# Performance work log

Measured on AMD Instinct MI355X. Metric: run time of the kernel, lower is better.

Reference implementation:

```python
import jax, jax.numpy as jnp
import numpy as np

SCALE_BASE = 512.0
GAMMA = 0.96875

def xpos(x, downscale=False):
    # x: (B, L, d). XPOS = rotary embedding with exponential position-dependent scale.
    B, L, d = x.shape
    half = d // 2
    scale_vec = (jnp.arange(0, d, 2, dtype=jnp.float32) + 0.4 * d) / (1.4 * d)  # (half,)
    pos = jnp.arange(L, dtype=jnp.float32)
    scale = scale_vec[None, :] ** (pos[:, None] / SCALE_BASE)  # (L, half)
    if downscale:
        scale = 1.0 / scale
    inv_freq = 1.0 / (10000.0 ** (jnp.arange(half, dtype=jnp.float32) / half))
    sinusoid = pos[:, None] * inv_freq[None, :]  # (L, half)
    sin_s = jnp.repeat(jnp.sin(sinusoid) * scale, 2, axis=-1)  # duplicate_interleave -> (L, d)
    cos_s = jnp.repeat(jnp.cos(sinusoid) * scale, 2, axis=-1)
    x1, x2 = x[..., ::2], x[..., 1::2]
    rot = jnp.stack((-x2, x1), axis=-1).reshape(x.shape)  # rotate_every_two
    return x * cos_s + rot * sin_s

def decay_mask(L, gamma):
    n = jnp.arange(L)[:, None]
    m = jnp.arange(L)[None, :]
    diff = n - m
    expo = jnp.where(diff >= 0, diff, 0).astype(jnp.float32)
    return jnp.where(diff >= 0, gamma ** expo, 0.0)  # (L, L) causal decay

def setup_inputs() -> dict:
    key = jax.random.key(0)
    kx, kq, kk, kv = jax.random.split(key, 4)
    B, L, H = 4, 2048, 1024
    hs = 1024  # head_size == v_dim
    X = jax.random.normal(kx, (B, L, H), dtype=jnp.float32)
    W_Q = jax.random.normal(kq, (H, hs), dtype=jnp.float32) / H
    W_K = jax.random.normal(kk, (H, hs), dtype=jnp.float32) / H
    W_V = jax.random.normal(kv, (H, hs), dtype=jnp.float32) / H
    return {"X": X, "W_Q": W_Q, "W_K": W_K, "W_V": W_V}

def reference(X, W_Q, W_K, W_V):
    L = X.shape[1]
    Q = xpos(X @ W_Q)
    K = xpos(X @ W_K, downscale=True)
    V = X @ W_V
    D = decay_mask(L, GAMMA)
    ret = jnp.einsum('bnd,bmd->bnm', Q, K) * D[None]  # (B, L, L)
    return ret @ V
```

## Files before the change

### kernel.cpp

```cpp
#include <hip/hip_runtime.h>
#include <cmath>

typedef __attribute__((ext_vector_type(8))) short short8;
typedef __attribute__((ext_vector_type(4))) short short4v;
typedef __attribute__((ext_vector_type(16))) float floatx16;
typedef __attribute__((ext_vector_type(4))) int int4v;
typedef unsigned short ushort_t;

#define LSEQ   2048
#define DMODEL 1024
#define BM 128
#define BN 128
#define BK 64
#define TPAD 136

#define L2GAMMA (-0.045803595f)
#define L2E4_512 (0.0259525632f)

__device__ __forceinline__ ushort_t f2b(float x) {
    union { float f; unsigned u; } v; v.f = x;
    unsigned r = v.u + 0x7fffu + ((v.u >> 16) & 1u);
    return (ushort_t)(r >> 16);
}

#define GLOAD_LDS16(gptr, lptr)                                                     \
    __builtin_amdgcn_global_load_lds(                                               \
        (const __attribute__((address_space(1))) unsigned int*)(gptr),              \
        (__attribute__((address_space(3))) unsigned int*)(lptr), 16, 0, 0)

#define DSR(d, a, o) \
    asm volatile("ds_read_b128 %0, %1 offset:" o : "=v"(d) : "v"(a))

__device__ __forceinline__ short8 as_s8(int4v v) {
    return __builtin_bit_cast(short8, v);
}
#define MFMA_B16 __builtin_amdgcn_mfma_f32_32x32x16_bf16

__device__ __forceinline__ void gemm_core(
    const ushort_t* __restrict__ Ag, int lda, int aRow0,
    const ushort_t* __restrict__ Bg, int ldb, int bRow0,
    int kDepth, ushort_t* As, ushort_t* Bs, floatx16 acc[2][2])
{
    const int tid  = threadIdx.x;
    const int wave = tid >> 6, lane = tid & 63;
    const int wm = wave >> 1, wn = wave & 1;
    const int l31 = lane & 31, half = lane >> 5;
    const int srow = lane >> 3;
    const int scol = ((lane & 7) ^ srow) * 8;

    const ushort_t* ap[4];
    const ushort_t* bp[4];
    #pragma unroll
    for (int L = 0; L < 4; ++L) {
        int r = (wave * 4 + L) * 8 + srow;
        ap[L] = Ag + (size_t)(aRow0 + r) * lda + scol;
        bp[L] = Bg + (size_t)(bRow0 + r) * ldb + scol;
    }
    const int ldst = (lane >> 3) * BK + (lane & 7) * 8;

    for (int k0 = 0; k0 < kDepth; k0 += BK) {
        __syncthreads();
        #pragma unroll
        for (int L = 0; L < 4; ++L) {
            GLOAD_LDS16(ap[L], As + (wave * 4 + L) * (8 * BK) + ldst);
            GLOAD_LDS16(bp[L], Bs + (wave * 4 + L) * (8 * BK) + ldst);
            ap[L] += BK; bp[L] += BK;
        }
        __syncthreads();

        #pragma unroll
        for (int ks = 0; ks < 4; ++ks) {
            const int ch = ((ks * 2 + half) ^ (l31 & 7)) * 8;
            short8 a0 = *(const short8*)(As + (wm * 64      + l31) * BK + ch);
            short8 a1 = *(const short8*)(As + (wm * 64 + 32 + l31) * BK + ch);
            short8 b0 = *(const short8*)(Bs + (wn * 64      + l31) * BK + ch);
            short8 b1 = *(const short8*)(Bs + (wn * 64 + 32 + l31) * BK + ch);
            acc[0][0] = MFMA_B16(a0, b0, acc[0][0], 0, 0, 0);
            acc[0][1] = MFMA_B16(a0, b1, acc[0][1], 0, 0, 0);
            acc[1][0] = MFMA_B16(a1, b0, acc[1][0], 0, 0, 0);
            acc[1][1] = MFMA_B16(a1, b1, acc[1][1], 0, 0, 0);
        }
    }
}

__global__ __launch_bounds__(256) void xpos_table_kernel(float2* __restrict__ T)
{
    int idx = blockIdx.x * 256 + threadIdx.x;
    int l = idx & 2047;
    int p = (idx >> 11) & 511;
    int mode = idx >> 20;
    float sv = (2.0f * (float)p + 409.6f) * (1.0f / 1433.6f);
    float coeff = log2f(sv) * (1.0f / 512.0f) + L2GAMMA;
    float invf = exp2f(-(float)p * L2E4_512);
    float lf = (float)l;
    float s, c;
    sincosf(lf * invf, &s, &c);
    float g = exp2f((mode == 0 ? lf : -lf) * coeff);
    T[idx] = make_float2(c * g, s * g);
}

__global__ __launch_bounds__(256) void cast_x_kernel(
    const float4* __restrict__ X, short4v* __restrict__ Xb, int n4)
{
    int i = blockIdx.x * 256 + threadIdx.x;
    if (i < n4) {
        float4 v = X[i];
        short4v o;
        o.x = (short)f2b(v.x); o.y = (short)f2b(v.y);
        o.z = (short)f2b(v.z); o.w = (short)f2b(v.w);
        Xb[i] = o;
    }
}

__global__ __launch_bounds__(256) void wtrans_kernel(
    const float* __restrict__ Wq, const float* __restrict__ Wk,
    const float* __restrict__ Wv, ushort_t* __restrict__ Wt)
{
    const float* W = blockIdx.z == 0 ? Wq : blockIdx.z == 1 ? Wk : Wv;
    ushort_t* O = Wt + (size_t)blockIdx.z * (DMODEL * DMODEL);
    __shared__ float t[32][33];
    const int x = threadIdx.x & 31, y = (threadIdx.x >> 5) * 4;
    const int k0 = blockIdx.y * 32, n0 = blockIdx.x * 32;
    #pragma unroll
    for (int j = 0; j < 4; ++j)
        t[y + j][x] = W[(size_t)(k0 + y + j) * DMODEL + n0 + x];
    __syncthreads();
    #pragma unroll
    for (int j = 0; j < 4; ++j)
        O[(size_t)(n0 + y + j) * DMODEL + k0 + x] = f2b(t[x][y + j]);
}

__global__ __launch_bounds__(256, 4) void qkv_kernel(
    const ushort_t* __restrict__ Xb, const ushort_t* __restrict__ Wt,
    const float2* __restrict__ Tab,
    ushort_t* __restrict__ Q, ushort_t* __restrict__ Ko, ushort_t* __restrict__ Vt)
{
    __shared__ ushort_t smem[128 * TPAD];
    ushort_t* As = smem;
    ushort_t* Bs = smem + BM * BK;

    const int lin = blockIdx.x;
    const int inner = lin & 63;
    const int sup = lin >> 6;
    const int c = (sup % 3) * 8 + (inner & 7);
    const int r = (sup / 3) * 8 + (inner >> 3);
    const int mode = c >> 3;
    const int c0 = (c & 7) * BN;
    const int row0 = r * BM;

    floatx16 acc[2][2] = {};
    gemm_core(Xb, DMODEL, row0,
              Wt + (size_t)mode * (DMODEL * DMODEL), DMODEL, c0,
              DMODEL, As, Bs, acc);

    const int wave = threadIdx.x >> 6, lane = threadIdx.x & 63;
    const int wm = wave >> 1, wn = wave & 1;
    const int l31 = lane & 31, half = lane >> 5;
    const int rBase = row0 + wm * 64 + 4 * half;
    const int cBase = c0 + wn * 64 + l31;

    if (mode == 2) {
        const int colL0 = wn * 64 + l31;
        const int rowL0 = wm * 64 + 4 * half;
        __syncthreads();
        #pragma unroll
        for (int mi = 0; mi < 2; ++mi)
            #pragma unroll
            for (int ni = 0; ni < 2; ++ni)
                #pragma unroll
                for (int rg = 0; rg < 4; ++rg) {
                    short4v pk;
                    pk.x = (short)f2b(acc[mi][ni][rg * 4 + 0]);
                    pk.y = (short)f2b(acc[mi][ni][rg * 4 + 1]);
                    pk.z = (short)f2b(acc[mi][ni][rg * 4 + 2]);
                    pk.w = (short)f2b(acc[mi][ni][rg * 4 + 3]);
                    *(short4v*)(smem + (colL0 + ni * 32) * TPAD
                                     + rowL0 + mi * 32 + 8 * rg) = pk;
                }
        __syncthreads();
        const int t = threadIdx.x;
        const int colV = c0 + (t >> 1);
        const int lhalf = (t & 1) * 64;
        const int b = row0 >> 11, lpos0 = (row0 & 2047) + lhalf;
        #pragma unroll
        for (int i = 0; i < 8; ++i) {
            short8 vv = *(const short8*)(smem + (t >> 1) * TPAD + lhalf + i * 8);
            *(short8*)(Vt + (size_t)b * (LSEQ * DMODEL)
                          + (size_t)colV * LSEQ + lpos0 + i * 8) = vv;
        }
    } else {
        ushort_t* O = (mode == 0) ? Q : Ko;
        const float2* Tm = Tab + (size_t)mode * (512 * 2048);
        #pragma unroll
        for (int ni = 0; ni < 2; ++ni) {
            int col = cBase + ni * 32;
            const float2* tp = Tm + ((size_t)(col >> 1) << 11);
            #pragma unroll
            for (int mi = 0; mi < 2; ++mi)
                #pragma unroll
                for (int rg = 0; rg < 4; ++rg) {
                    int l0 = (rBase + mi * 32 + 8 * rg) & 2047;
                    float4 t01 = *(const float4*)(tp + l0);
                    float4 t23 = *(const float4*)(tp + l0 + 2);
                    float cs[8] = {t01.x, t01.y, t01.z, t01.w,
                                   t23.x, t23.y, t23.z, t23.w};
                    #pragma unroll
                    for (int q = 0; q < 4; ++q) {
                        int row = rBase + mi * 32 + 8 * rg + q;
                        float cc = cs[2 * q], ss = cs[2 * q + 1];
                        float v  = acc[mi][ni][rg * 4 + q];
                        float pv = __shfl_xor(v, 1);
                        float res = (lane & 1) ? fmaf(v, cc, pv * ss)
                                               : fmaf(v, cc, -pv * ss);
                        O[(size_t)row * DMODEL + col] = f2b(res);
                    }
                }
        }
    }
}

__global__ __launch_bounds__(512, 2) void qkv256_kernel(
    const ushort_t* __restrict__ Xb, const ushort_t* __restrict__ Wt,
    const float2* __restrict__ Tab,
    ushort_t* __restrict__ Q, ushort_t* __restrict__ Ko, ushort_t* __restrict__ Vt)
{
    extern __shared__ ushort_t smem[];
    const int tid  = threadIdx.x;
    const int wave = tid >> 6, lane = tid & 63;
    const int wm = wave >> 2, wn = wave & 3;
    const int l31 = lane & 31, half = lane >> 5;
    const int xl  = l31 & 7;

    const int nwg = gridDim.x;
    const int cpx = nwg >> 3;
    const int orig = blockIdx.x;
    const int wg = (orig & 7) * cpx + (orig >> 3);
    const int sup = wg >> 4, inner = wg & 15;
    const int ct = (sup % 3) * 4 + (inner & 3);
    const int rt = (sup / 3) * 4 + (inner >> 2);
    const int mode = ct >> 2;
    const int row0 = rt << 8;
    const int c0m  = (ct & 3) << 8;

    const char* gA = (const char*)Xb;
    const char* gB = (const char*)(Wt + (size_t)mode * (DMODEL * DMODEL));

    const int t8 = tid >> 3;
    const int scol = (((tid & 7) ^ (t8 & 7)) << 3);
    unsigned oA0  = (unsigned)(((row0 + t8) * DMODEL + scol) * 2);
    unsigned oA0b = oA0 + 64  * DMODEL * 2;
    unsigned oA1  = oA0 + 128 * DMODEL * 2;
    unsigned oA1b = oA0 + 192 * DMODEL * 2;
    unsigned oB0  = (unsigned)(((c0m + t8) * DMODEL + scol) * 2);
    unsigned oB0b = oB0 + 64  * DMODEL * 2;
    unsigned oB1  = oB0 + 128 * DMODEL * 2;
    unsigned oB1b = oB0 + 192 * DMODEL * 2;

    char* ldsT = (char*)smem + tid * 16;
    int stg = 0;

    int vaA[4], vaB[4];
    #pragma unroll
    for (int ks = 0; ks < 4; ++ks) {
        const int swz = (((ks * 2 + half) ^ xl) << 4);
        vaA[ks] = wm * 16384 + l31 * 128 + swz;
        vaB[ks] = 65536 + (wn >> 1) * 16384 + ((wn & 1) * 64 + l31) * 128 + swz;
    }

    GLOAD_LDS16(gA + oA0,  ldsT);                  GLOAD_LDS16(gA + oA0b, ldsT + 8192);
    GLOAD_LDS16(gA + oA1,  ldsT + 16384);          GLOAD_LDS16(gA + oA1b, ldsT + 16384 + 8192);
    GLOAD_LDS16(gB + oB0,  ldsT + 65536);          GLOAD_LDS16(gB + oB0b, ldsT + 65536 + 8192);
    GLOAD_LDS16(gB + oB1,  ldsT + 65536 + 16384);  GLOAD_LDS16(gB + oB1b, ldsT + 65536 + 16384 + 8192);
    oA0 += 128; oA0b += 128; oA1 += 128; oA1b += 128;
    oB0 += 128; oB0b += 128; oB1 += 128; oB1b += 128;
    GLOAD_LDS16(gA + oA0, ldsT + 32768);           GLOAD_LDS16(gA + oA0b, ldsT + 32768 + 8192);
    oA0 += 128; oA0b += 128;
    asm volatile("s_waitcnt vmcnt(2)" ::: "memory");
    __builtin_amdgcn_s_barrier();

    floatx16 acc[4][2] = {};
    int4v a0[2][4], a2[2][4], b0[4], b1[4];

    for (int j = 0; j < 16; ++j) {
        const int nstg = stg ^ 32768;

        #pragma unroll
        for (int ks = 0; ks < 4; ++ks) {
            DSR(a0[0][ks], vaA[ks], "0");
            DSR(a0[1][ks], vaA[ks], "4096");
            DSR(b0[ks],    vaB[ks], "0");
        }
        GLOAD_LDS16(gA + oA1,  ldsT + nstg + 16384);
        GLOAD_LDS16(gA + oA1b, ldsT + nstg + 16384 + 8192);
        oA1 += 128; oA1b += 128;
        GLOAD_LDS16(gB + oB0,  ldsT + nstg + 65536);
        GLOAD_LDS16(gB + oB0b, ldsT + nstg + 65536 + 8192);
        oB0 += 128; oB0b += 128;
        asm volatile("s_waitcnt lgkmcnt(0)" ::: "memory");
        __builtin_amdgcn_sched_barrier(0);
        __builtin_amdgcn_s_setprio(1);
        #pragma unroll
        for (int ks = 0; ks < 4; ++ks) {
            acc[0][0] = MFMA_B16(as_s8(a0[0][ks]), as_s8(b0[ks]), acc[0][0], 0, 0, 0);
            acc[1][0] = MFMA_B16(as_s8(a0[1][ks]), as_s8(b0[ks]), acc[1][0], 0, 0, 0);
        }
        __builtin_amdgcn_s_setprio(0);

        #pragma unroll
        for (int ks = 0; ks < 4; ++ks)
            DSR(b1[ks], vaB[ks], "4096");
        GLOAD_LDS16(gB + oB1,  ldsT + nstg + 65536 + 16384);
        GLOAD_LDS16(gB + oB1b, ldsT + nstg + 65536 + 16384 + 8192);
        oB1 += 128; oB1b += 128;
        asm volatile("s_waitcnt lgkmcnt(0)" ::: "memory");
        __builtin_amdgcn_sched_barrier(0);
        __builtin_amdgcn_s_setprio(1);
        #pragma unroll
        for (int ks = 0; ks < 4; ++ks) {
            acc[0][1] = MFMA_B16(as_s8(a0[0][ks]), as_s8(b1[ks]), acc[0][1], 0, 0, 0);
            acc[1][1] = MFMA_B16(as_s8(a0[1][ks]), as_s8(b1[ks]), acc[1][1], 0, 0, 0);
        }
        __builtin_amdgcn_s_setprio(0);

        #pragma unroll
        for (int ks = 0; ks < 4; ++ks) {
            DSR(a2[0][ks], vaA[ks], "8192");
            DSR(a2[1][ks], vaA[ks], "12288");
        }
        asm volatile("s_waitcnt lgkmcnt(0)" ::: "memory");
        __builtin_amdgcn_sched_barrier(0);
        __builtin_amdgcn_s_setprio(1);
        #pragma unroll
        for (int ks = 0; ks < 4; ++ks) {
            acc[2][0] = MFMA_B16(as_s8(a2[0][ks]), as_s8(b0[ks]), acc[2][0], 0, 0, 0);
            acc[3][0] = MFMA_B16(as_s8(a2[1][ks]), as_s8(b0[ks]), acc[3][0], 0, 0, 0);
        }
        __builtin_amdgcn_s_setprio(0);

        __builtin_amdgcn_s_barrier();

        GLOAD_LDS16(gA + oA0,  ldsT + stg);
        GLOAD_LDS16(gA + oA0b, ldsT + stg + 8192);
        oA0 += 128; oA0b += 128;
        __builtin_amdgcn_s_setprio(1);
        #pragma unroll
        for (int ks = 0; ks < 4; ++ks) {
            acc[2][1] = MFMA_B16(as_s8(a2[0][ks]), as_s8(b1[ks]), acc[2][1], 0, 0, 0);
            acc[3][1] = MFMA_B16(as_s8(a2[1][ks]), as_s8(b1[ks]), acc[3][1], 0, 0, 0);
        }
        __builtin_amdgcn_s_setprio(0);
        asm volatile("s_waitcnt vmcnt(2)" ::: "memory");
        __builtin_amdgcn_s_barrier();

        stg ^= 32768;
        #pragma unroll
        for (int ks = 0; ks < 4; ++ks) { vaA[ks] ^= 32768; vaB[ks] ^= 32768; }
    }

    const int rB = row0 + wm * 128 + 4 * half;
    const int cB = c0m + wn * 64 + l31;

    if (mode < 2) {
        ushort_t* O = (mode == 0) ? Q : Ko;
        const float2* Tm = Tab + (size_t)mode * (512 * 2048);
        #pragma unroll
        for (int n = 0; n < 2; ++n) {
            const int col = cB + n * 32;
            const float2* tp = Tm + ((size_t)(col >> 1) << 11);
            #pragma unroll
            for (int m = 0; m < 4; ++m)
                #pragma unroll
                for (int rg = 0; rg < 4; ++rg) {
                    const int row = rB + m * 32 + 8 * rg;
                    const int l0 = row & 2047;
                    float4 t01 = *(const float4*)(tp + l0);
                    float4 t23 = *(const float4*)(tp + l0 + 2);
                    float cs[8] = {t01.x, t01.y, t01.z, t01.w,
                                   t23.x, t23.y, t23.z, t23.w};
                    #pragma unroll
                    for (int q = 0; q < 4; ++q) {
                        float v  = acc[m][n][rg * 4 + q];
                        float pv = __shfl_xor(v, 1);
                        float cc = cs[2 * q], ss = cs[2 * q + 1];
                        float res = (lane & 1) ? fmaf(v, cc, pv * ss)
                                               : fmaf(v, cc, -pv * ss);
                        O[(size_t)(row + q) * DMODEL + col] = f2b(res);
                    }
                }
        }
    } else {
        __syncthreads();
        const int bidx = row0 >> 11, lpos0 = row0 & 2047;
        #pragma unroll
        for (int ph = 0; ph < 2; ++ph) {
            if ((wn >> 1) == ph) {
                const int colL = (wn & 1) * 64 + l31;
                const int rowL = wm * 128 + 4 * half;
                #pragma unroll
                for (int m = 0; m < 4; ++m)
                    #pragma unroll
                    for (int n = 0; n < 2; ++n)
                        #pragma unroll
                        for (int rg = 0; rg < 4; ++rg) {
                            short4v pk;
                            pk.x = (short)f2b(acc[m][n][rg * 4 + 0]);
                            pk.y = (short)f2b(acc[m][n][rg * 4 + 1]);
                            pk.z = (short)f2b(acc[m][n][rg * 4 + 2]);
                            pk.w = (short)f2b(acc[m][n][rg * 4 + 3]);
                            *(short4v*)(smem + (size_t)(colL + n * 32) * 264
                                             + rowL + m * 32 + 8 * rg) = pk;
                        }
            }
            __syncthreads();
            const int colV = c0m + ph * 128 + (tid >> 2);
            const int qtr  = tid & 3;
            #pragma unroll
            for (int i = 0; i < 8; ++i) {
                short8 vv = *(const short8*)(smem + (size_t)(tid >> 2) * 264
                                                  + qtr * 64 + i * 8);
                *(short8*)(Vt + (size_t)bidx * (LSEQ * DMODEL)
                              + (size_t)colV * LSEQ + lpos0 + qtr * 64 + i * 8) = vv;
            }
            __syncthreads();
        }
    }
    asm volatile("s_waitcnt vmcnt(0)" ::: "memory");
}

__global__ __launch_bounds__(256, 4) void score_kernel(
    const ushort_t* __restrict__ Q, const ushort_t* __restrict__ Kc,
    ushort_t* __restrict__ S)
{
    const int t = blockIdx.x, z = blockIdx.z;
    int bi, bj;
    if (t < 3) { bi = (t > 0); bj = t - (t > 0); }
    else { int u = t - 3; bi = 2 + u / 3; bj = bi - 2 + u % 3; }

    __shared__ ushort_t As[BM * BK], Bs[BN * BK];
    floatx16 acc[2][2] = {};
    const size_t zoff = (size_t)z * (LSEQ * DMODEL);
    gemm_core(Q + zoff, DMODEL, bi * BM, Kc + zoff, DMODEL, bj * BN,
              DMODEL, As, Bs, acc);

    const int wave = threadIdx.x >> 6, lane = threadIdx.x & 63;
    const int wm = wave >> 1, wn = wave & 1;
    const int l31 = lane & 31, half = lane >> 5;
    const int nBase = bi * BM + wm * 64 + 4 * half;
    const int mBase = bj * BN + wn * 64 + l31;
    ushort_t* Sz = S + (size_t)z * LSEQ * LSEQ;
    #pragma unroll
    for (int mi = 0; mi < 2; ++mi)
        #pragma unroll
        for (int ni = 0; ni < 2; ++ni) {
            int m = mBase + ni * 32;
            #pragma unroll
            for (int rg = 0; rg < 4; ++rg)
                #pragma unroll
                for (int q = 0; q < 4; ++q) {
                    int n = nBase + mi * 32 + 8 * rg + q;
                    Sz[(size_t)n * LSEQ + m] =
                        (m <= n) ? f2b(acc[mi][ni][rg * 4 + q]) : (ushort_t)0;
                }
        }
}

__global__ __launch_bounds__(256, 4) void av_kernel(
    const ushort_t* __restrict__ S, const ushort_t* __restrict__ Vt,
    float* __restrict__ Out)
{
    const int bx = blockIdx.x, bi = blockIdx.y, z = blockIdx.z;
    const int kLo = (bi >= 2) ? (bi - 2) * BM : 0;
    const int kW  = (bi + 1) * BM - kLo;
    __shared__ ushort_t As[BM * BK], Bs[BN * BK];
    floatx16 acc[2][2] = {};
    gemm_core(S + (size_t)z * LSEQ * LSEQ + kLo, LSEQ, bi * BM,
              Vt + (size_t)z * (LSEQ * DMODEL) + kLo, LSEQ, bx * BN,
              kW, As, Bs, acc);

    const int wave = threadIdx.x >> 6, lane = threadIdx.x & 63;
    const int wm = wave >> 1, wn = wave & 1;
    const int l31 = lane & 31, half = lane >> 5;
    const int rBase = bi * BM + wm * 64 + 4 * half;
    const int cBase = bx * BN + wn * 64 + l31;
    float* Oz = Out + (size_t)z * (LSEQ * DMODEL);
    #pragma unroll
    for (int mi = 0; mi < 2; ++mi)
        #pragma unroll
        for (int ni = 0; ni < 2; ++ni)
            #pragma unroll
            for (int rg = 0; rg < 4; ++rg)
                #pragma unroll
                for (int q = 0; q < 4; ++q)
                    Oz[(size_t)(rBase + mi * 32 + 8 * rg + q) * DMODEL
                       + cBase + ni * 32] = acc[mi][ni][rg * 4 + q];
}

extern "C" void kernel_launch(void* const* d_in, const int* in_sizes, int n_in,
                              void* d_out, int out_size, void* d_ws, size_t ws_size,
                              hipStream_t stream)
{
    const float* X  = (const float*)d_in[0];
    const float* Wq = (const float*)d_in[1];
    const float* Wk = (const float*)d_in[2];
    const float* Wv = (const float*)d_in[3];
    float* out = (float*)d_out;

    const size_t LH  = (size_t)LSEQ * DMODEL;
    const size_t WSZ = (size_t)DMODEL * DMODEL;
    const size_t SSZ = (size_t)LSEQ * LSEQ;
    const size_t TABN = (size_t)2 * 512 * 2048;

    size_t need4 = TABN * 8 + 2 * (3 * WSZ + 4 * (4 * LH + SSZ));
    const int bs = (ws_size >= need4) ? 4 : 1;

    float2* Tab = (float2*)d_ws;
    ushort_t* ws16 = (ushort_t*)(Tab + TABN);
    ushort_t* Wt = ws16;
    ushort_t* Xb = Wt + 3 * WSZ;
    ushort_t* Q  = Xb + (size_t)bs * LH;
    ushort_t* Kb = Q  + (size_t)bs * LH;
    ushort_t* Vt = Kb + (size_t)bs * LH;
    ushort_t* S  = Vt + (size_t)bs * LH;

    static int qkv256_ok = -1;
    if (qkv256_ok < 0) {
        hipError_t e = hipFuncSetAttribute(
            reinterpret_cast<const void*>(qkv256_kernel),
            hipFuncAttributeMaxDynamicSharedMemorySize, 131072);
        qkv256_ok = (e == hipSuccess) ? 1 : 0;
    }

    xpos_table_kernel<<<dim3(TABN / 256), 256, 0, stream>>>(Tab);
    wtrans_kernel<<<dim3(32, 32, 3), 256, 0, stream>>>(Wq, Wk, Wv, Wt);

    for (int p = 0; p < 4 / bs; ++p) {
        const float* Xp = X + (size_t)p * bs * LH;
        cast_x_kernel<<<dim3(bs * 2048), 256, 0, stream>>>(
            (const float4*)Xp, (short4v*)Xb, bs * (int)(LH / 4));
        if (qkv256_ok)
            qkv256_kernel<<<dim3(96 * bs), 512, 131072, stream>>>(
                Xb, Wt, Tab, Q, Kb, Vt);
        else
            qkv_kernel<<<dim3(24 * bs * 16), 256, 0, stream>>>(
                Xb, Wt, Tab, Q, Kb, Vt);
        score_kernel<<<dim3(45, 1, bs), 256, 0, stream>>>(Q, Kb, S);
        av_kernel<<<dim3(8, 16, bs), 256, 0, stream>>>(S, Vt,
            out + (size_t)p * bs * LH);
    }
}
```

Baseline: 215.6 us.

## Software-pipeline LDS fragment reads across k-steps in projection GEMM loop

Reorders the projection GEMM main loop so each k-step loads all A and B fragments in one phase, with two register sets that alternate. The next k-step's LDS reads are issued before the current step's MFMAs, and partial lgkmcnt(6) waits replace full drains. This is meant to hide LDS read latency behind matrix math and to cut the fragment registers in use. The first fragment read of the next tile is issued after the end-of-iteration barrier, and the final vmcnt drain moves to right after the loop.

```diff
diff --git a/kernel.cpp b/kernel.cpp
--- a/kernel.cpp
+++ b/kernel.cpp
@@ -267,6 +267,35 @@
         vaB[ks] = 65536 + (wn >> 1) * 16384 + ((wn & 1) * 64 + l31) * 128 + swz;
     }
 
+#define WAITL6 do { asm volatile("s_waitcnt lgkmcnt(6)" ::: "memory"); \
+                    __builtin_amdgcn_sched_barrier(0); } while (0)
+#define WAITL0 do { asm volatile("s_waitcnt lgkmcnt(0)" ::: "memory"); \
+                    __builtin_amdgcn_sched_barrier(0); } while (0)
+
+#define PH_ISSUE(dA0, dA1, dA2, dA3, dB0, dB1, kn)  \
+    do {                                             \
+        DSR(dA0, vaA[kn], "0");                      \
+        DSR(dA1, vaA[kn], "4096");                   \
+        DSR(dA2, vaA[kn], "8192");                   \
+        DSR(dA3, vaA[kn], "12288");                  \
+        DSR(dB0, vaB[kn], "0");                      \
+        DSR(dB1, vaB[kn], "4096");                   \
+    } while (0)
+
+#define PH_MFMA(A0_, A1_, A2_, A3_, B0_, B1_)                                  \
+    do {                                                                       \
+        __builtin_amdgcn_s_setprio(1);                                         \
+        acc[0][0] = MFMA_B16(as_s8(A0_), as_s8(B0_), acc[0][0], 0, 0, 0);      \
+        acc[0][1] = MFMA_B16(as_s8(A0_), as_s8(B1_), acc[0][1], 0, 0, 0);      \
+        acc[1][0] = MFMA_B16(as_s8(A1_), as_s8(B0_), acc[1][0], 0, 0, 0);      \
+        acc[1][1] = MFMA_B16(as_s8(A1_), as_s8(B1_), acc[1][1], 0, 0, 0);      \
+        acc[2][0] = MFMA_B16(as_s8(A2_), as_s8(B0_), acc[2][0], 0, 0, 0);      \
+        acc[2][1] = MFMA_B16(as_s8(A2_), as_s8(B1_), acc[2][1], 0, 0, 0);      \
+        acc[3][0] = MFMA_B16(as_s8(A3_), as_s8(B0_), acc[3][0], 0, 0, 0);      \
+        acc[3][1] = MFMA_B16(as_s8(A3_), as_s8(B1_), acc[3][1], 0, 0, 0);      \
+        __builtin_amdgcn_s_setprio(0);                                         \
+    } while (0)
+
     GLOAD_LDS16(gA + oA0,  ldsT);                  GLOAD_LDS16(gA + oA0b, ldsT + 8192);
     GLOAD_LDS16(gA + oA1,  ldsT + 16384);          GLOAD_LDS16(gA + oA1b, ldsT + 16384 + 8192);
     GLOAD_LDS16(gB + oB0,  ldsT + 65536);          GLOAD_LDS16(gB + oB0b, ldsT + 65536 + 8192);
@@ -279,83 +308,52 @@
     __builtin_amdgcn_s_barrier();
 
     floatx16 acc[4][2] = {};
-    int4v a0[2][4], a2[2][4], b0[4], b1[4];
+    int4v sA0, sA1, sA2, sA3, sB0, sB1;
+    int4v tA0, tA1, tA2, tA3, tB0, tB1;
+
+    PH_ISSUE(sA0, sA1, sA2, sA3, sB0, sB1, 0);
 
     for (int j = 0; j < 16; ++j) {
         const int nstg = stg ^ 32768;
 
-        #pragma unroll
-        for (int ks = 0; ks < 4; ++ks) {
-            DSR(a0[0][ks], vaA[ks], "0");
-            DSR(a0[1][ks], vaA[ks], "4096");
-            DSR(b0[ks],    vaB[ks], "0");
-        }
         GLOAD_LDS16(gA + oA1,  ldsT + nstg + 16384);
         GLOAD_LDS16(gA + oA1b, ldsT + nstg + 16384 + 8192);
         oA1 += 128; oA1b += 128;
         GLOAD_LDS16(gB + oB0,  ldsT + nstg + 65536);
         GLOAD_LDS16(gB + oB0b, ldsT + nstg + 65536 + 8192);
         oB0 += 128; oB0b += 128;
-        asm volatile("s_waitcnt lgkmcnt(0)" ::: "memory");
-        __builtin_amdgcn_sched_barrier(0);
-        __builtin_amdgcn_s_setprio(1);
-        #pragma unroll
-        for (int ks = 0; ks < 4; ++ks) {
-            acc[0][0] = MFMA_B16(as_s8(a0[0][ks]), as_s8(b0[ks]), acc[0][0], 0, 0, 0);
-            acc[1][0] = MFMA_B16(as_s8(a0[1][ks]), as_s8(b0[ks]), acc[1][0], 0, 0, 0);
-        }
-        __builtin_amdgcn_s_setprio(0);
-
-        #pragma unroll
-        for (int ks = 0; ks < 4; ++ks)
-            DSR(b1[ks], vaB[ks], "4096");
+        PH_ISSUE(tA0, tA1, tA2, tA3, tB0, tB1, 1);
+        WAITL6;
+        PH_MFMA(sA0, sA1, sA2, sA3, sB0, sB1);
+
         GLOAD_LDS16(gB + oB1,  ldsT + nstg + 65536 + 16384);
         GLOAD_LDS16(gB + oB1b, ldsT + nstg + 65536 + 16384 + 8192);
         oB1 += 128; oB1b += 128;
-        asm volatile("s_waitcnt lgkmcnt(0)" ::: "memory");
-        __builtin_amdgcn_sched_barrier(0);
-        __builtin_amdgcn_s_setprio(1);
-        #pragma unroll
-        for (int ks = 0; ks < 4; ++ks) {
-            acc[0][1] = MFMA_B16(as_s8(a0[0][ks]), as_s8(b1[ks]), acc[0][1], 0, 0, 0);
-            acc[1][1] = MFMA_B16(as_s8(a0[1][ks]), as_s8(b1[ks]), acc[1][1], 0, 0, 0);
-        }
-        __builtin_amdgcn_s_setprio(0);
-
-        #pragma unroll
-        for (int ks = 0; ks < 4; ++ks) {
-            DSR(a2[0][ks], vaA[ks], "8192");
-            DSR(a2[1][ks], vaA[ks], "12288");
-        }
-        asm volatile("s_waitcnt lgkmcnt(0)" ::: "memory");
-        __builtin_amdgcn_sched_barrier(0);
-        __builtin_amdgcn_s_setprio(1);
-        #pragma unroll
-        for (int ks = 0; ks < 4; ++ks) {
-            acc[2][0] = MFMA_B16(as_s8(a2[0][ks]), as_s8(b0[ks]), acc[2][0], 0, 0, 0);
-            acc[3][0] = MFMA_B16(as_s8(a2[1][ks]), as_s8(b0[ks]), acc[3][0], 0, 0, 0);
-        }
-        __builtin_amdgcn_s_setprio(0);
+        PH_ISSUE(sA0, sA1, sA2, sA3, sB0, sB1, 2);
+        WAITL6;
+        PH_MFMA(tA0, tA1, tA2, tA3, tB0, tB1);
+
+        PH_ISSUE(tA0, tA1, tA2, tA3, tB0, tB1, 3);
+        WAITL6;
+        PH_MFMA(sA0, sA1, sA2, sA3, sB0, sB1);
+
+        WAITL0;
+        PH_MFMA(tA0, tA1, tA2, tA3, tB0, tB1);
 
         __builtin_amdgcn_s_barrier();
-
         GLOAD_LDS16(gA + oA0,  ldsT + stg);
         GLOAD_LDS16(gA + oA0b, ldsT + stg + 8192);
         oA0 += 128; oA0b += 128;
-        __builtin_amdgcn_s_setprio(1);
-        #pragma unroll
-        for (int ks = 0; ks < 4; ++ks) {
-            acc[2][1] = MFMA_B16(as_s8(a2[0][ks]), as_s8(b1[ks]), acc[2][1], 0, 0, 0);
-            acc[3][1] = MFMA_B16(as_s8(a2[1][ks]), as_s8(b1[ks]), acc[3][1], 0, 0, 0);
-        }
-        __builtin_amdgcn_s_setprio(0);
         asm volatile("s_waitcnt vmcnt(2)" ::: "memory");
         __builtin_amdgcn_s_barrier();
 
         stg ^= 32768;
         #pragma unroll
         for (int ks = 0; ks < 4; ++ks) { vaA[ks] ^= 32768; vaB[ks] ^= 32768; }
-    }
+
+        PH_ISSUE(sA0, sA1, sA2, sA3, sB0, sB1, 0);
+    }
+    asm volatile("s_waitcnt vmcnt(0)" ::: "memory");
 
     const int rB = row0 + wm * 128 + 4 * half;
     const int cB = c0m + wn * 64 + l31;
@@ -424,7 +422,10 @@
             __syncthreads();
         }
     }
-    asm volatile("s_waitcnt vmcnt(0)" ::: "memory");
+#undef WAITL6
+#undef WAITL0
+#undef PH_ISSUE
+#undef PH_MFMA
 }
 
 __global__ __launch_bounds__(256, 4) void score_kernel(
```

Measured after the change: 208.2 us. 1.04x faster.
